# Kernel tuning notes

Measured on AMD Instinct MI355X. Metric: run time of the kernel, lower is better.

Reference implementation:

```python
import jax, jax.numpy as jnp
import numpy as np
from jax import lax

THR = 0.0
NMS_SIZE = 5
PAD = NMS_SIZE // 2
B, C, H, W = 8, 1, 2048, 2048
# Upper bound on number of surviving peaks: ~1/(2*25) of pixels pass in
# expectation for iid noise; B*H*W//8 is a very safe static cap.
MAX_PEAKS = (B * H * W) // 8


def max_filter(x):
    # torch MaxPool2d(kernel=5, stride=1, padding=2) == max reduce_window
    # with -inf padding, same spatial output shape.
    return lax.reduce_window(
        x, -jnp.inf, lax.max,
        window_dimensions=(1, 1, NMS_SIZE, NMS_SIZE),
        window_strides=(1, 1, 1, 1),
        padding=[(0, 0), (0, 0), (PAD, PAD), (PAD, PAD)],
    )


def setup_inputs() -> dict:
    key = jax.random.key(0)
    scores = jax.random.normal(key, (B, C, H, W), dtype=jnp.float32)
    return {"scores": scores}


def reference(scores):
    # maxima = (scores == maxpool(scores)) & (scores > thr)
    maxima = (scores == max_filter(scores)) & (scores > THR)
    # torch: maxima.nonzero().t()[2:4] -> [2, K] rows = (h, w) coords.
    # jit-safe: fixed-size nonzero, padded with -1 for absent entries.
    idx = jnp.nonzero(maxima, size=MAX_PEAKS, fill_value=-1)
    return jnp.stack([idx[2], idx[3]])  # [2, MAX_PEAKS]
```

## Files before the change

### kernel.cpp

```cpp
#include <hip/hip_runtime.h>
#include <math.h>

#define IMG_W 2048
#define IMG_H 2048
#define BATCH 8
#define MAX_PEAKS ((BATCH * IMG_H * IMG_W) / 8)
#define NWORDS (BATCH * IMG_H * IMG_W / 32)
#define ROWSW 32
#define NFILL 2048

__device__ __forceinline__ void load_row(const float* __restrict__ colp,
                                         const float* __restrict__ ecolp,
                                         int gr, bool leftHalf, bool evalid,
                                         float4& nv, float2& ne) {
    const float NEG = -INFINITY;
    int rc = gr < 0 ? 0 : (gr > IMG_H - 1 ? IMG_H - 1 : gr);
    size_t off = (size_t)rc * IMG_W;
    float4 v = *(const float4*)(colp + off);
    float4 ev = *(const float4*)(ecolp + off);
    bool rv = ((unsigned)gr < IMG_H);
    bool ok = rv && evalid;
    float ex = leftHalf ? ev.z : ev.x;
    float ey = leftHalf ? ev.w : ev.y;
    nv.x = rv ? v.x : NEG;
    nv.y = rv ? v.y : NEG;
    nv.z = rv ? v.z : NEG;
    nv.w = rv ? v.w : NEG;
    ne.x = ok ? ex : NEG;
    ne.y = ok ? ey : NEG;
}

__global__ __launch_bounds__(256, 4) void nms_mask(const float* __restrict__ scores,
                                                   unsigned* __restrict__ words,
                                                   unsigned* __restrict__ bsum2) {
    const int t = threadIdx.x;
    const int lane = t & 63;
    const int wv = t >> 6;
    const int b = blockIdx.x;
    const int img = b >> 7;
    const int rem = b & 127;
    const int strip = rem >> 4;
    const int chunk = rem & 15;
    const int r0 = chunk * 128 + wv * ROWSW;
    const int c0 = strip * 256;
    const int cl = c0 + lane * 4;
    const size_t imgBase = (size_t)img * (IMG_H * IMG_W);

    const float* colp = scores + imgBase + cl;
    const bool leftHalf = (lane < 32);
    const bool isL = (lane == 0), isR = (lane == 63);
    int ecol = leftHalf ? (c0 - 4) : (c0 + 256);
    const bool evalid = ((unsigned)ecol < IMG_W);
    int ecolC = evalid ? ecol : c0;
    const float* ecolp = scores + imgBase + ecolC;

    float4 ring[8];
    float2 ringE[8];

#pragma unroll
    for (int m = 0; m < 4; ++m)
        load_row(colp, ecolp, r0 - 2 + m, leftHalf, evalid, ring[m], ringE[m]);

    unsigned cnt = 0;
    const int shamt = (lane & 7) * 4;
    size_t wIdx = (size_t)(img * IMG_H + r0) * (IMG_W / 32) + strip * 8 + (lane >> 3);
    const int cb0 = (img * IMG_H + r0) >> 4;

#pragma unroll 1
    for (int i8 = 0; i8 < ROWSW / 8; ++i8) {
#pragma unroll
        for (int u = 0; u < 8; ++u) {
            const int gr = r0 + i8 * 8 + u + 2;
            load_row(colp, ecolp, gr, leftHalf, evalid,
                     ring[(u + 4) & 7], ringE[(u + 4) & 7]);

            const float4 w0 = ring[u & 7];
            const float4 w1 = ring[(u + 1) & 7];
            const float4 mid = ring[(u + 2) & 7];
            const float4 w3 = ring[(u + 3) & 7];
            const float4 w4 = ring[(u + 4) & 7];
            float vmx = fmaxf(fmaxf(fmaxf(w0.x, w1.x), fmaxf(mid.x, w3.x)), w4.x);
            float vmy = fmaxf(fmaxf(fmaxf(w0.y, w1.y), fmaxf(mid.y, w3.y)), w4.y);
            float vmz = fmaxf(fmaxf(fmaxf(w0.z, w1.z), fmaxf(mid.z, w3.z)), w4.z);
            float vmw = fmaxf(fmaxf(fmaxf(w0.w, w1.w), fmaxf(mid.w, w3.w)), w4.w);
            const float2 e0 = ringE[u & 7];
            const float2 e1 = ringE[(u + 1) & 7];
            const float2 e2 = ringE[(u + 2) & 7];
            const float2 e3 = ringE[(u + 3) & 7];
            const float2 e4 = ringE[(u + 4) & 7];
            float vex = fmaxf(fmaxf(fmaxf(e0.x, e1.x), fmaxf(e2.x, e3.x)), e4.x);
            float vey = fmaxf(fmaxf(fmaxf(e0.y, e1.y), fmaxf(e2.y, e3.y)), e4.y);

            float A = __shfl_up(vmz, 1);
            float B = __shfl_up(vmw, 1);
            float C = __shfl_down(vmx, 1);
            float D = __shfl_down(vmy, 1);
            if (isL) { A = vex; B = vey; }
            if (isR) { C = vex; D = vey; }

            float t12 = fmaxf(vmy, vmz);
            float m02 = fmaxf(vmx, t12);
            float m03 = fmaxf(m02, vmw);
            float m13 = fmaxf(t12, vmw);
            float h0 = fmaxf(fmaxf(A, B), m02);
            float h1 = fmaxf(B, m03);
            float h2 = fmaxf(m03, C);
            float h3 = fmaxf(m13, fmaxf(C, D));

            unsigned nib = 0;
            nib |= (mid.x > 0.0f && mid.x >= h0) ? 1u : 0u;
            nib |= (mid.y > 0.0f && mid.y >= h1) ? 2u : 0u;
            nib |= (mid.z > 0.0f && mid.z >= h2) ? 4u : 0u;
            nib |= (mid.w > 0.0f && mid.w >= h3) ? 8u : 0u;

            unsigned wd = nib << shamt;
            wd |= __shfl_xor(wd, 1);
            wd |= __shfl_xor(wd, 2);
            wd |= __shfl_xor(wd, 4);
            if ((lane & 7) == 0) {
                words[wIdx] = wd;
                cnt += __popc(wd);
            }
            wIdx += IMG_W / 32;
        }
        if (i8 & 1) {
            unsigned s = cnt;
            s += __shfl_xor(s, 1);
            s += __shfl_xor(s, 2);
            s += __shfl_xor(s, 4);
            s += __shfl_xor(s, 8);
            s += __shfl_xor(s, 16);
            s += __shfl_xor(s, 32);
            if (lane == 0) bsum2[(cb0 + (i8 >> 1)) * 8 + strip] = s;
            cnt = 0;
        }
    }
}

__global__ __launch_bounds__(256) void nms_scan(const unsigned* __restrict__ bsum2,
                                                unsigned* __restrict__ base) {
    __shared__ unsigned wtot[4];
    const int t = threadIdx.x;
    const int lane = t & 63, wid = t >> 6;
    const uint4* p = (const uint4*)(bsum2 + t * 32);
    unsigned c[4];
#pragma unroll
    for (int i = 0; i < 4; ++i) {
        uint4 a = p[2 * i], bq = p[2 * i + 1];
        c[i] = a.x + a.y + a.z + a.w + bq.x + bq.y + bq.z + bq.w;
    }
    unsigned s0 = c[0], s1 = s0 + c[1], s2 = s1 + c[2], ts = s2 + c[3];
    unsigned sc = ts;
#pragma unroll
    for (int d = 1; d < 64; d <<= 1) {
        unsigned o = __shfl_up(sc, d);
        if (lane >= d) sc += o;
    }
    if (lane == 63) wtot[wid] = sc;
    __syncthreads();
    unsigned wpre = 0;
#pragma unroll
    for (int k = 0; k < 4; ++k) wpre += (k < wid) ? wtot[k] : 0u;
    unsigned excl = wpre + sc - ts;
    ((uint4*)base)[t] = make_uint4(excl, excl + s0, excl + s1, excl + s2);
    if (t == 255) base[1024] = wpre + sc;
}

__global__ __launch_bounds__(256) void nms_compact(const unsigned* __restrict__ words,
                                                   const unsigned* __restrict__ base,
                                                   int* __restrict__ out) {
    const int t = threadIdx.x;
    const int b = blockIdx.x;
    if (b < 1024) {
        __shared__ unsigned wq[4];
        const int lane = t & 63, wid = t >> 6;
        uint4 q = ((const uint4*)(words + b * 1024))[t];
        unsigned wv[4] = {q.x, q.y, q.z, q.w};
        unsigned tsum = __popc(wv[0]) + __popc(wv[1]) + __popc(wv[2]) + __popc(wv[3]);
        unsigned sc = tsum;
#pragma unroll
        for (int d = 1; d < 64; d <<= 1) {
            unsigned o = __shfl_up(sc, d);
            if (lane >= d) sc += o;
        }
        if (lane == 63) wq[wid] = sc;
        __syncthreads();
        unsigned wpre = 0;
#pragma unroll
        for (int k = 0; k < 4; ++k) wpre += (k < wid) ? wq[k] : 0u;
        unsigned off = base[b] + wpre + sc - tsum;

        const unsigned gword0 = (unsigned)b * 1024u + (unsigned)t * 4u;
#pragma unroll
        for (int wi = 0; wi < 4; ++wi) {
            unsigned m = wv[wi];
            unsigned pbase = (gword0 + wi) << 5;
            while (m) {
                int bit = __builtin_ctz(m);
                m &= m - 1;
                unsigned ppix = pbase + (unsigned)bit;
                int hh = (int)((ppix >> 11) & 2047u);
                int ww = (int)(ppix & 2047u);
                if (off < (unsigned)MAX_PEAKS) {
                    out[off] = hh;
                    out[MAX_PEAKS + off] = ww;
                }
                ++off;
            }
        }
    } else {
        unsigned total = base[1024];
        if (total > (unsigned)MAX_PEAKS) total = MAX_PEAKS;
        unsigned tail = (unsigned)MAX_PEAKS - total;
        unsigned fb = (unsigned)(b - 1024);
        unsigned per = (tail + NFILL - 1) / NFILL;
        unsigned s = total + fb * per;
        unsigned e = s + per;
        if (e > (unsigned)MAX_PEAKS) e = MAX_PEAKS;
        for (unsigned k = s + t; k < e; k += 256) {
            out[k] = -1;
            out[MAX_PEAKS + k] = -1;
        }
    }
}

extern "C" void kernel_launch(void* const* d_in, const int* in_sizes, int n_in,
                              void* d_out, int out_size, void* d_ws, size_t ws_size,
                              hipStream_t stream) {
    const float* scores = (const float*)d_in[0];
    int* out = (int*)d_out;
    unsigned* words = (unsigned*)d_ws;
    unsigned* bsum2 = words + NWORDS;
    unsigned* base = bsum2 + 8192;

    nms_mask<<<1024, 256, 0, stream>>>(scores, words, bsum2);
    nms_scan<<<1, 256, 0, stream>>>(bsum2, base);
    nms_compact<<<1024 + NFILL, 256, 0, stream>>>(words, base, out);
}
```

Baseline: 212.4 us.

## Separable row-first max filter, drop scan kernel, vectorize fill

The mask kernel now computes the horizontal max per row once and keeps a rolling window of five horizontal results, instead of recomputing vertical maxima over a ring of raw rows. Halo handling uses pointer stepping with clamped advances, and each wave covers 16 rows with more blocks and a remapped block order. The separate single-block scan kernel is removed; each compact block sums the preceding block counts itself, trading a kernel launch for redundant prefix reads. The -1 tail fill uses int4 stores with scalar head and tail handling.

```diff
diff --git a/kernel.cpp b/kernel.cpp
--- a/kernel.cpp
+++ b/kernel.cpp
@@ -6,174 +6,159 @@
 #define BATCH 8
 #define MAX_PEAKS ((BATCH * IMG_H * IMG_W) / 8)
 #define NWORDS (BATCH * IMG_H * IMG_W / 32)
-#define ROWSW 32
 #define NFILL 2048
 
-__device__ __forceinline__ void load_row(const float* __restrict__ colp,
-                                         const float* __restrict__ ecolp,
-                                         int gr, bool leftHalf, bool evalid,
-                                         float4& nv, float2& ne) {
-    const float NEG = -INFINITY;
-    int rc = gr < 0 ? 0 : (gr > IMG_H - 1 ? IMG_H - 1 : gr);
-    size_t off = (size_t)rc * IMG_W;
-    float4 v = *(const float4*)(colp + off);
-    float4 ev = *(const float4*)(ecolp + off);
-    bool rv = ((unsigned)gr < IMG_H);
-    bool ok = rv && evalid;
-    float ex = leftHalf ? ev.z : ev.x;
-    float ey = leftHalf ? ev.w : ev.y;
-    nv.x = rv ? v.x : NEG;
-    nv.y = rv ? v.y : NEG;
-    nv.z = rv ? v.z : NEG;
-    nv.w = rv ? v.w : NEG;
-    ne.x = ok ? ex : NEG;
-    ne.y = ok ? ey : NEG;
-}
-
-__global__ __launch_bounds__(256, 4) void nms_mask(const float* __restrict__ scores,
+
+#define LOADR(RS, ES)                                                         \
+  {                                                                           \
+    RS = *(const float4*)p;                                                   \
+    const float2 _e = *(const float2*)pe;                                     \
+    ES.x = evalid ? _e.x : NEG;                                               \
+    ES.y = evalid ? _e.y : NEG;                                               \
+    const size_t stepB =                                                      \
+        ((unsigned)(xn - 1) < 2047u) ? (size_t)(IMG_W * 4) : (size_t)0;       \
+    p = (const float*)((const char*)p + stepB);                               \
+    pe = (const float*)((const char*)pe + stepB);                             \
+    ++xn;                                                                     \
+  }
+
+#define HMR(RS, ES, HS)                                                       \
+  {                                                                           \
+    float Av = __shfl_up(RS.z, 1);                                            \
+    float Bv = __shfl_up(RS.w, 1);                                            \
+    float Cv = __shfl_down(RS.x, 1);                                          \
+    float Dv = __shfl_down(RS.y, 1);                                          \
+    if (isL) { Av = ES.x; Bv = ES.y; }                                        \
+    if (isR) { Cv = ES.x; Dv = ES.y; }                                        \
+    const float t12 = fmaxf(RS.y, RS.z);                                      \
+    const float m02 = fmaxf(RS.x, t12);                                       \
+    const float m03 = fmaxf(m02, RS.w);                                       \
+    const float m13 = fmaxf(t12, RS.w);                                       \
+    HS.x = fmaxf(fmaxf(Av, Bv), m02);                                         \
+    HS.y = fmaxf(Bv, m03);                                                    \
+    HS.z = fmaxf(m03, Cv);                                                    \
+    HS.w = fmaxf(m13, fmaxf(Cv, Dv));                                         \
+  }
+
+#define OUTR(MR)                                                              \
+  {                                                                           \
+    const float mx = fmaxf(fmaxf(fmaxf(H0.x, H1.x), fmaxf(H2.x, H3.x)), H4.x);\
+    const float my = fmaxf(fmaxf(fmaxf(H0.y, H1.y), fmaxf(H2.y, H3.y)), H4.y);\
+    const float mz = fmaxf(fmaxf(fmaxf(H0.z, H1.z), fmaxf(H2.z, H3.z)), H4.z);\
+    const float mw = fmaxf(fmaxf(fmaxf(H0.w, H1.w), fmaxf(H2.w, H3.w)), H4.w);\
+    unsigned nib = 0;                                                         \
+    nib |= (MR.x > 0.0f && MR.x >= mx) ? 1u : 0u;                             \
+    nib |= (MR.y > 0.0f && MR.y >= my) ? 2u : 0u;                             \
+    nib |= (MR.z > 0.0f && MR.z >= mz) ? 4u : 0u;                             \
+    nib |= (MR.w > 0.0f && MR.w >= mw) ? 8u : 0u;                             \
+    unsigned wd = nib << shamt;                                               \
+    wd |= __shfl_xor(wd, 1);                                                  \
+    wd |= __shfl_xor(wd, 2);                                                  \
+    wd |= __shfl_xor(wd, 4);                                                  \
+    if ((lane & 7) == 0) {                                                    \
+      words[wIdx] = wd;                                                       \
+      cnt += __popc(wd);                                                      \
+    }                                                                         \
+    wIdx += IMG_W / 32;                                                       \
+  }
+
+__global__ __launch_bounds__(256, 6) void nms_mask(const float* __restrict__ scores,
                                                    unsigned* __restrict__ words,
                                                    unsigned* __restrict__ bsum2) {
     const int t = threadIdx.x;
     const int lane = t & 63;
     const int wv = t >> 6;
     const int b = blockIdx.x;
-    const int img = b >> 7;
-    const int rem = b & 127;
-    const int strip = rem >> 4;
-    const int chunk = rem & 15;
-    const int r0 = chunk * 128 + wv * ROWSW;
+    const int L = (b >> 3) + (b & 7) * 256;
+    const int img = L >> 8;
+    const int rem = L & 255;
+    const int strip = rem >> 5;
+    const int chunk = rem & 31;
+    const int r0 = chunk * 64 + wv * 16;
     const int c0 = strip * 256;
     const int cl = c0 + lane * 4;
-    const size_t imgBase = (size_t)img * (IMG_H * IMG_W);
-
-    const float* colp = scores + imgBase + cl;
+    const size_t imgBase = (size_t)img * ((size_t)IMG_H * IMG_W);
+    const float NEG = -INFINITY;
+
     const bool leftHalf = (lane < 32);
     const bool isL = (lane == 0), isR = (lane == 63);
-    int ecol = leftHalf ? (c0 - 4) : (c0 + 256);
-    const bool evalid = ((unsigned)ecol < IMG_W);
-    int ecolC = evalid ? ecol : c0;
-    const float* ecolp = scores + imgBase + ecolC;
-
-    float4 ring[8];
-    float2 ringE[8];
-
-#pragma unroll
-    for (int m = 0; m < 4; ++m)
-        load_row(colp, ecolp, r0 - 2 + m, leftHalf, evalid, ring[m], ringE[m]);
+    const int ecol2 = leftHalf ? (c0 - 2) : (c0 + 256);
+    const bool evalid = ((unsigned)ecol2 < (unsigned)IMG_W);
+    const int ecol2C = evalid ? ecol2 : c0;
+
+    const int rstart = (r0 - 2) < 0 ? 0 : (r0 - 2);
+    const float* p = scores + imgBase + (size_t)rstart * IMG_W + cl;
+    const float* pe = scores + imgBase + (size_t)rstart * IMG_W + ecol2C;
+    int xn = r0 - 1;
+
+    float4 R0, R1, R2, R3;
+    float4 H0, H1, H2, H3, H4;
+    float2 E0, E1;
 
     unsigned cnt = 0;
     const int shamt = (lane & 7) * 4;
     size_t wIdx = (size_t)(img * IMG_H + r0) * (IMG_W / 32) + strip * 8 + (lane >> 3);
     const int cb0 = (img * IMG_H + r0) >> 4;
 
-#pragma unroll 1
-    for (int i8 = 0; i8 < ROWSW / 8; ++i8) {
-#pragma unroll
-        for (int u = 0; u < 8; ++u) {
-            const int gr = r0 + i8 * 8 + u + 2;
-            load_row(colp, ecolp, gr, leftHalf, evalid,
-                     ring[(u + 4) & 7], ringE[(u + 4) & 7]);
-
-            const float4 w0 = ring[u & 7];
-            const float4 w1 = ring[(u + 1) & 7];
-            const float4 mid = ring[(u + 2) & 7];
-            const float4 w3 = ring[(u + 3) & 7];
-            const float4 w4 = ring[(u + 4) & 7];
-            float vmx = fmaxf(fmaxf(fmaxf(w0.x, w1.x), fmaxf(mid.x, w3.x)), w4.x);
-            float vmy = fmaxf(fmaxf(fmaxf(w0.y, w1.y), fmaxf(mid.y, w3.y)), w4.y);
-            float vmz = fmaxf(fmaxf(fmaxf(w0.z, w1.z), fmaxf(mid.z, w3.z)), w4.z);
-            float vmw = fmaxf(fmaxf(fmaxf(w0.w, w1.w), fmaxf(mid.w, w3.w)), w4.w);
-            const float2 e0 = ringE[u & 7];
-            const float2 e1 = ringE[(u + 1) & 7];
-            const float2 e2 = ringE[(u + 2) & 7];
-            const float2 e3 = ringE[(u + 3) & 7];
-            const float2 e4 = ringE[(u + 4) & 7];
-            float vex = fmaxf(fmaxf(fmaxf(e0.x, e1.x), fmaxf(e2.x, e3.x)), e4.x);
-            float vey = fmaxf(fmaxf(fmaxf(e0.y, e1.y), fmaxf(e2.y, e3.y)), e4.y);
-
-            float A = __shfl_up(vmz, 1);
-            float B = __shfl_up(vmw, 1);
-            float C = __shfl_down(vmx, 1);
-            float D = __shfl_down(vmy, 1);
-            if (isL) { A = vex; B = vey; }
-            if (isR) { C = vex; D = vey; }
-
-            float t12 = fmaxf(vmy, vmz);
-            float m02 = fmaxf(vmx, t12);
-            float m03 = fmaxf(m02, vmw);
-            float m13 = fmaxf(t12, vmw);
-            float h0 = fmaxf(fmaxf(A, B), m02);
-            float h1 = fmaxf(B, m03);
-            float h2 = fmaxf(m03, C);
-            float h3 = fmaxf(m13, fmaxf(C, D));
-
-            unsigned nib = 0;
-            nib |= (mid.x > 0.0f && mid.x >= h0) ? 1u : 0u;
-            nib |= (mid.y > 0.0f && mid.y >= h1) ? 2u : 0u;
-            nib |= (mid.z > 0.0f && mid.z >= h2) ? 4u : 0u;
-            nib |= (mid.w > 0.0f && mid.w >= h3) ? 8u : 0u;
-
-            unsigned wd = nib << shamt;
-            wd |= __shfl_xor(wd, 1);
-            wd |= __shfl_xor(wd, 2);
-            wd |= __shfl_xor(wd, 4);
-            if ((lane & 7) == 0) {
-                words[wIdx] = wd;
-                cnt += __popc(wd);
-            }
-            wIdx += IMG_W / 32;
-        }
-        if (i8 & 1) {
-            unsigned s = cnt;
-            s += __shfl_xor(s, 1);
-            s += __shfl_xor(s, 2);
-            s += __shfl_xor(s, 4);
-            s += __shfl_xor(s, 8);
-            s += __shfl_xor(s, 16);
-            s += __shfl_xor(s, 32);
-            if (lane == 0) bsum2[(cb0 + (i8 >> 1)) * 8 + strip] = s;
-            cnt = 0;
-        }
-    }
+    LOADR(R0, E0);
+    LOADR(R1, E1); HMR(R0, E0, H0);
+    LOADR(R2, E0); HMR(R1, E1, H1);
+    LOADR(R3, E1); HMR(R2, E0, H2);
+    LOADR(R0, E0); HMR(R3, E1, H3);
+    LOADR(R1, E1); HMR(R0, E0, H4); OUTR(R2);
+    LOADR(R2, E0); HMR(R1, E1, H0); OUTR(R3);
+    LOADR(R3, E1); HMR(R2, E0, H1); OUTR(R0);
+    LOADR(R0, E0); HMR(R3, E1, H2); OUTR(R1);
+    LOADR(R1, E1); HMR(R0, E0, H3); OUTR(R2);
+    LOADR(R2, E0); HMR(R1, E1, H4); OUTR(R3);
+    LOADR(R3, E1); HMR(R2, E0, H0); OUTR(R0);
+    LOADR(R0, E0); HMR(R3, E1, H1); OUTR(R1);
+    LOADR(R1, E1); HMR(R0, E0, H2); OUTR(R2);
+    LOADR(R2, E0); HMR(R1, E1, H3); OUTR(R3);
+    LOADR(R3, E1); HMR(R2, E0, H4); OUTR(R0);
+    LOADR(R0, E0); HMR(R3, E1, H0); OUTR(R1);
+    LOADR(R1, E1); HMR(R0, E0, H1); OUTR(R2);
+    LOADR(R2, E0); HMR(R1, E1, H2); OUTR(R3);
+    LOADR(R3, E1); HMR(R2, E0, H3); OUTR(R0);
+                   HMR(R3, E1, H4); OUTR(R1);
+
+    unsigned s = cnt;
+    s += __shfl_xor(s, 1);
+    s += __shfl_xor(s, 2);
+    s += __shfl_xor(s, 4);
+    s += __shfl_xor(s, 8);
+    s += __shfl_xor(s, 16);
+    s += __shfl_xor(s, 32);
+    if (lane == 0) bsum2[cb0 * 8 + strip] = s;
 }
 
-__global__ __launch_bounds__(256) void nms_scan(const unsigned* __restrict__ bsum2,
-                                                unsigned* __restrict__ base) {
-    __shared__ unsigned wtot[4];
-    const int t = threadIdx.x;
-    const int lane = t & 63, wid = t >> 6;
-    const uint4* p = (const uint4*)(bsum2 + t * 32);
-    unsigned c[4];
-#pragma unroll
-    for (int i = 0; i < 4; ++i) {
-        uint4 a = p[2 * i], bq = p[2 * i + 1];
-        c[i] = a.x + a.y + a.z + a.w + bq.x + bq.y + bq.z + bq.w;
-    }
-    unsigned s0 = c[0], s1 = s0 + c[1], s2 = s1 + c[2], ts = s2 + c[3];
-    unsigned sc = ts;
-#pragma unroll
-    for (int d = 1; d < 64; d <<= 1) {
-        unsigned o = __shfl_up(sc, d);
-        if (lane >= d) sc += o;
-    }
-    if (lane == 63) wtot[wid] = sc;
-    __syncthreads();
-    unsigned wpre = 0;
-#pragma unroll
-    for (int k = 0; k < 4; ++k) wpre += (k < wid) ? wtot[k] : 0u;
-    unsigned excl = wpre + sc - ts;
-    ((uint4*)base)[t] = make_uint4(excl, excl + s0, excl + s1, excl + s2);
-    if (t == 255) base[1024] = wpre + sc;
-}
-
 __global__ __launch_bounds__(256) void nms_compact(const unsigned* __restrict__ words,
-                                                   const unsigned* __restrict__ base,
+                                                   const unsigned* __restrict__ bsum2,
                                                    int* __restrict__ out) {
     const int t = threadIdx.x;
     const int b = blockIdx.x;
+    const int lane = t & 63, wid = t >> 6;
+    __shared__ unsigned sred[4];
+    __shared__ unsigned wq[4];
+
+    const int limq = ((b < 1024) ? (b * 8) : 8192) >> 2;
+    unsigned acc = 0;
+    const uint4* p4 = (const uint4*)bsum2;
+    for (int i = t; i < limq; i += 256) {
+        uint4 a = p4[i];
+        acc += a.x + a.y + a.z + a.w;
+    }
+    acc += __shfl_xor(acc, 1);
+    acc += __shfl_xor(acc, 2);
+    acc += __shfl_xor(acc, 4);
+    acc += __shfl_xor(acc, 8);
+    acc += __shfl_xor(acc, 16);
+    acc += __shfl_xor(acc, 32);
+    if (lane == 0) sred[wid] = acc;
+    __syncthreads();
+    const unsigned basev = sred[0] + sred[1] + sred[2] + sred[3];
+
     if (b < 1024) {
-        __shared__ unsigned wq[4];
-        const int lane = t & 63, wid = t >> 6;
         uint4 q = ((const uint4*)(words + b * 1024))[t];
         unsigned wv[4] = {q.x, q.y, q.z, q.w};
         unsigned tsum = __popc(wv[0]) + __popc(wv[1]) + __popc(wv[2]) + __popc(wv[3]);
@@ -188,7 +173,7 @@
         unsigned wpre = 0;
 #pragma unroll
         for (int k = 0; k < 4; ++k) wpre += (k < wid) ? wq[k] : 0u;
-        unsigned off = base[b] + wpre + sc - tsum;
+        unsigned off = basev + wpre + sc - tsum;
 
         const unsigned gword0 = (unsigned)b * 1024u + (unsigned)t * 4u;
 #pragma unroll
@@ -209,17 +194,31 @@
             }
         }
     } else {
-        unsigned total = base[1024];
+        unsigned total = basev;
         if (total > (unsigned)MAX_PEAKS) total = MAX_PEAKS;
         unsigned tail = (unsigned)MAX_PEAKS - total;
         unsigned fb = (unsigned)(b - 1024);
         unsigned per = (tail + NFILL - 1) / NFILL;
         unsigned s = total + fb * per;
         unsigned e = s + per;
+        if (s > (unsigned)MAX_PEAKS) s = MAX_PEAKS;
         if (e > (unsigned)MAX_PEAKS) e = MAX_PEAKS;
-        for (unsigned k = s + t; k < e; k += 256) {
-            out[k] = -1;
-            out[MAX_PEAKS + k] = -1;
+        unsigned a = (s + 3u) & ~3u;
+        if (a > e) a = e;
+        unsigned e4 = e & ~3u;
+        if (e4 < a) e4 = a;
+        if ((unsigned)t < a - s) {
+            out[s + t] = -1;
+            out[MAX_PEAKS + s + t] = -1;
+        }
+        const int4 m4 = make_int4(-1, -1, -1, -1);
+        for (unsigned k = a / 4 + t; k < e4 / 4; k += 256) {
+            ((int4*)out)[k] = m4;
+            ((int4*)(out + MAX_PEAKS))[k] = m4;
+        }
+        if ((unsigned)t < e - e4) {
+            out[e4 + t] = -1;
+            out[MAX_PEAKS + e4 + t] = -1;
         }
     }
 }
@@ -231,9 +230,7 @@
     int* out = (int*)d_out;
     unsigned* words = (unsigned*)d_ws;
     unsigned* bsum2 = words + NWORDS;
-    unsigned* base = bsum2 + 8192;
-
-    nms_mask<<<1024, 256, 0, stream>>>(scores, words, bsum2);
-    nms_scan<<<1, 256, 0, stream>>>(bsum2, base);
-    nms_compact<<<1024 + NFILL, 256, 0, stream>>>(words, base, out);
+
+    nms_mask<<<2048, 256, 0, stream>>>(scores, words, bsum2);
+    nms_compact<<<1024 + NFILL, 256, 0, stream>>>(words, bsum2, out);
 }
```

After: 216.7 us. +2.0%, slower.
